# Performance work log

Hardware: AMD Instinct MI355X
Metric: run time of the kernel (lower is better)

The kernel has to match this reference:

```python
import jax, jax.numpy as jnp
import numpy as np

N_NODES = 50000
N_EDGES = 1600000
IN_CH = 128
OUT_SZ = 64


def setup_inputs() -> dict:
    key = jax.random.key(0)
    ks = jax.random.split(key, 10)
    seq = jax.random.normal(ks[0], (N_NODES, IN_CH), dtype=jnp.float32)
    edge_index = jax.random.randint(ks[1], (2, N_EDGES), 0, N_NODES, dtype=jnp.int64)
    s = 1.0 / np.sqrt(IN_CH)
    W_seq = jax.random.uniform(ks[2], (OUT_SZ, IN_CH), jnp.float32, -s, s)
    so = 1.0 / np.sqrt(OUT_SZ)
    w_f1 = jax.random.uniform(ks[3], (OUT_SZ,), jnp.float32, -so, so)
    b_f1 = jax.random.uniform(ks[4], (), jnp.float32, -so, so)
    w_f2 = jax.random.uniform(ks[5], (OUT_SZ,), jnp.float32, -so, so)
    b_f2 = jax.random.uniform(ks[6], (), jnp.float32, -so, so)
    bias = jnp.zeros((OUT_SZ,), jnp.float32)
    W_res = jax.random.uniform(ks[7], (OUT_SZ, IN_CH), jnp.float32, -s, s)
    b_res = jax.random.uniform(ks[8], (OUT_SZ,), jnp.float32, -s, s)
    return {"seq": seq, "edge_index": edge_index, "W_seq": W_seq,
            "w_f1": w_f1, "b_f1": b_f1, "w_f2": w_f2, "b_f2": b_f2,
            "bias": bias, "W_res": W_res, "b_res": b_res}


def reference(seq, edge_index, W_seq, w_f1, b_f1, w_f2, b_f2, bias, W_res, b_res):
    # seq: (N, in_ch); 1x1 conv == linear map per node
    seq_fts = jnp.einsum('ni,oi->no', seq, W_seq)          # (N, out)
    f1 = seq_fts @ w_f1 + b_f1                              # (N,)
    f2 = seq_fts @ w_f2 + b_f2                              # (N,)
    src, dst = edge_index[0], edge_index[1]
    e = jax.nn.leaky_relu(f1[src] + f2[dst], negative_slope=0.01)  # (E,)
    # NOTE: global softmax over all edges, as in the original (not per-node)
    coefs = jax.nn.softmax(e)                               # (E,)
    weighted = coefs[:, None] * seq_fts[dst]                # (E, out)
    vals = jax.ops.segment_sum(weighted, src, num_segments=seq.shape[0])  # (N, out)
    ret = vals + bias
    # residual: in_channel != out_sz -> 1x1 conv with bias
    ret = ret + jnp.einsum('ni,oi->no', seq, W_res) + b_res
    return jax.nn.elu(ret)
```

## Files before the change

kernel.cpp:

```cpp
#include <hip/hip_runtime.h>
#include <hip/hip_bf16.h>
#include <hip/hip_fp8.h>
#include <math.h>

#define N_NODES 50000
#define N_EDGES 1600000
#define IN_CH 128
#define OUT_SZ 64
#define N_TILES 3125

#define NBK 196
#define EPB 4096
#define NBL 391
#define CAP 10240

typedef short bf16x8 __attribute__((ext_vector_type(8)));
typedef float f32x4  __attribute__((ext_vector_type(4)));

__device__ __forceinline__ unsigned fenc(float x) {
    unsigned u = __float_as_uint(x);
    return (u & 0x80000000u) ? ~u : (u | 0x80000000u);
}
__device__ __forceinline__ float fdec(unsigned u) {
    return __uint_as_float((u & 0x80000000u) ? (u & 0x7fffffffu) : ~u);
}

__device__ __forceinline__ short bfbits(float x) {
    union { __hip_bfloat16 h; short s; } u;
    u.h = __float2bfloat16(x);
    return u.s;
}
__device__ __forceinline__ bf16x8 pack8(const float* f) {
    bf16x8 r;
#pragma unroll
    for (int j = 0; j < 8; ++j) r[j] = bfbits(f[j]);
    return r;
}

__global__ __launch_bounds__(256) void k_zero(unsigned* pmax1, unsigned* pmax2,
                                              float* psum, unsigned* bcur) {
    const int t = threadIdx.x;
    if (t < NBK) bcur[t * 16] = (unsigned)t * CAP;
    if (t == 0) { *pmax1 = 0u; *pmax2 = 0u; *psum = 0.0f; }
}

__global__ __launch_bounds__(256) void k_fused(
    const int* __restrict__ ei, unsigned* __restrict__ bcur,
    unsigned* __restrict__ pairs,
    const float* __restrict__ seq, const float* __restrict__ Wseq,
    const float* __restrict__ Wres, const float* __restrict__ wf1,
    const float* __restrict__ bf1, const float* __restrict__ wf2,
    const float* __restrict__ bf2, const float* __restrict__ bias,
    const float* __restrict__ bres,
    __hip_fp8_e4m3* __restrict__ sfp8, float* __restrict__ f1,
    float* __restrict__ f2, unsigned* pmax1, unsigned* pmax2,
    float* __restrict__ out)
{
    __shared__ unsigned buf[EPB];
    __shared__ unsigned hcnt[NBK];
    __shared__ unsigned hoff[NBK];
    __shared__ bf16x8 WL[2048];
    __shared__ float smax[8];
    const int t = threadIdx.x;

    if (blockIdx.x < NBL) {
        const int blk = blockIdx.x;
        if (t < NBK) hcnt[t] = 0u;
        __syncthreads();
#pragma unroll
        for (int k = 0; k < 4; ++k) {
            int idx4 = k * 256 + t;
            int e4 = blk * EPB + idx4 * 4;
            if (e4 < N_EDGES) {
                int4 s = *(const int4*)(ei + e4);
                int4 d = *(const int4*)(ei + N_EDGES + e4);
                buf[k * 1024 + 0 * 256 + t] = ((unsigned)s.x << 16) | (unsigned)d.x;
                buf[k * 1024 + 1 * 256 + t] = ((unsigned)s.y << 16) | (unsigned)d.y;
                buf[k * 1024 + 2 * 256 + t] = ((unsigned)s.z << 16) | (unsigned)d.z;
                buf[k * 1024 + 3 * 256 + t] = ((unsigned)s.w << 16) | (unsigned)d.w;
                atomicAdd(&hcnt[s.x >> 8], 1u);
                atomicAdd(&hcnt[s.y >> 8], 1u);
                atomicAdd(&hcnt[s.z >> 8], 1u);
                atomicAdd(&hcnt[s.w >> 8], 1u);
            }
        }
        __syncthreads();
        if (t < NBK) {
            unsigned c = hcnt[t];
            hoff[t] = c ? atomicAdd(&bcur[t * 16], c) : 0u;
            hcnt[t] = 0u;
        }
        __syncthreads();
#pragma unroll
        for (int k = 0; k < 4; ++k) {
            int idx4 = k * 256 + t;
            int e4 = blk * EPB + idx4 * 4;
            if (e4 < N_EDGES) {
#pragma unroll
                for (int j = 0; j < 4; ++j) {
                    unsigned p = buf[k * 1024 + j * 256 + t];
                    unsigned b = p >> 24;
                    unsigned lp = atomicAdd(&hcnt[b], 1u);
                    pairs[hoff[b] + lp] = p;
                }
            }
        }
        return;
    }

#pragma unroll
    for (int j = 0; j < 8; ++j) {
        int idx = t + j * 256;
        int ct = idx >> 8;
        int ks = (idx >> 6) & 3;
        int li = idx & 63;
        int c = ct * 16 + (li & 15);
        int k0 = ks * 32 + (li >> 4) * 8;
        const float* src = (c < 64) ? (Wseq + c * IN_CH + k0)
                                    : (Wres + (c - 64) * IN_CH + k0);
        float tmp[8];
        *(float4*)tmp = *(const float4*)src;
        *(float4*)(tmp + 4) = *(const float4*)(src + 4);
        WL[idx] = pack8(tmp);
    }
    __syncthreads();

    const int l = t & 63;
    const int wv = t >> 6;
    const int tile = (int)(blockIdx.x - NBL) * 4 + wv;
    const bool active = tile < N_TILES;
    float mx1 = -3.0e38f, mx2 = -3.0e38f;

    if (active) {
        const int row = tile * 16 + (l & 15);
        const int kbase = (l >> 4) * 8;
        f32x4 acc[8];
#pragma unroll
        for (int ct = 0; ct < 8; ++ct) acc[ct] = (f32x4){0.f, 0.f, 0.f, 0.f};

#pragma unroll
        for (int ks = 0; ks < 4; ++ks) {
            const float* ap = seq + (size_t)row * IN_CH + ks * 32 + kbase;
            float tmp[8];
            *(float4*)tmp = *(const float4*)ap;
            *(float4*)(tmp + 4) = *(const float4*)(ap + 4);
            bf16x8 af = pack8(tmp);
#pragma unroll
            for (int ct = 0; ct < 8; ++ct)
                acc[ct] = __builtin_amdgcn_mfma_f32_16x16x32_bf16(
                    af, WL[(ct * 4 + ks) * 64 + l], acc[ct], 0, 0, 0);
        }

        const int n0 = tile * 16;
        float w1v[4], w2v[4], bb[4];
#pragma unroll
        for (int ct = 0; ct < 4; ++ct) {
            int oc = ct * 16 + (l & 15);
            w1v[ct] = wf1[oc];
            w2v[ct] = wf2[oc];
            bb[ct] = bias[oc] + bres[oc];
        }
        const float B1 = bf1[0], B2 = bf2[0];
#pragma unroll
        for (int r = 0; r < 4; ++r) {
            int node = n0 + (l >> 4) * 4 + r;
            size_t o = (size_t)node * 64 + (l & 15);
#pragma unroll
            for (int ct = 0; ct < 4; ++ct) {
                sfp8[o + ct * 16] = __hip_fp8_e4m3(acc[ct][r]);
                out[o + ct * 16] = acc[ct + 4][r] + bb[ct];
            }
            float t1 = acc[0][r] * w1v[0] + acc[1][r] * w1v[1]
                     + acc[2][r] * w1v[2] + acc[3][r] * w1v[3];
            float t2 = acc[0][r] * w2v[0] + acc[1][r] * w2v[1]
                     + acc[2][r] * w2v[2] + acc[3][r] * w2v[3];
#pragma unroll
            for (int m = 8; m; m >>= 1) {
                t1 += __shfl_xor(t1, m);
                t2 += __shfl_xor(t2, m);
            }
            if ((l & 15) == 0) {
                float F1 = t1 + B1, F2 = t2 + B2;
                f1[node] = F1;
                f2[node] = F2;
                mx1 = fmaxf(mx1, F1);
                mx2 = fmaxf(mx2, F2);
            }
        }
    }

    mx1 = fmaxf(mx1, __shfl_xor(mx1, 16)); mx1 = fmaxf(mx1, __shfl_xor(mx1, 32));
    mx2 = fmaxf(mx2, __shfl_xor(mx2, 16)); mx2 = fmaxf(mx2, __shfl_xor(mx2, 32));
    if (l == 0) { smax[wv] = mx1; smax[4 + wv] = mx2; }
    __syncthreads();
    if (t == 0) {
        atomicMax(pmax1, fenc(fmaxf(fmaxf(smax[0], smax[1]), fmaxf(smax[2], smax[3]))));
        atomicMax(pmax2, fenc(fmaxf(fmaxf(smax[4], smax[5]), fmaxf(smax[6], smax[7]))));
    }
}

__global__ __launch_bounds__(1024) void k_sortsum(
    const unsigned* __restrict__ pairs, const unsigned* __restrict__ bcur,
    const float* __restrict__ f1, const float* __restrict__ f2,
    const unsigned* __restrict__ pmax1, const unsigned* __restrict__ pmax2,
    unsigned* __restrict__ offs, unsigned* __restrict__ offsE,
    unsigned* __restrict__ sPair, float* psum)
{
    __shared__ unsigned cur[256];
    __shared__ unsigned bs[256];
    __shared__ float f1loc[256];
    __shared__ float red[16];
    const int t = threadIdx.x;
    const int b = blockIdx.x;
    const int nbase = b << 8;
    const unsigned eb = (unsigned)b * CAP;
    const unsigned ee = bcur[b * 16];

    if (t < 256) {
        cur[t] = 0u;
        int n = nbase + t;
        f1loc[t] = (n < N_NODES) ? f1[n] : 0.f;
    }
    __syncthreads();

    for (unsigned i = eb + t; i < ee; i += 1024)
        atomicAdd(&cur[(pairs[i] >> 16) & 255u], 1u);
    __syncthreads();

    unsigned v = (t < 256) ? cur[t] : 0u;
    if (t < 256) bs[t] = v;
    __syncthreads();
    for (int off = 1; off < 256; off <<= 1) {
        unsigned w = (t >= off && t < 256) ? bs[t - off] : 0u;
        __syncthreads();
        if (t < 256) bs[t] += w;
        __syncthreads();
    }
    if (t < 256) {
        unsigned o = eb + (bs[t] - v);
        int n = nbase + t;
        if (n < N_NODES) { offs[n] = o; offsE[n] = o + v; }
        cur[t] = o;
    }
    __syncthreads();

    float M = fdec(*pmax1) + fdec(*pmax2);
    M = (M > 0.f) ? M : 0.01f * M;
    float ls = 0.f;
    for (unsigned i = eb + t; i < ee; i += 1024) {
        unsigned p = pairs[i];
        unsigned li = (p >> 16) & 255u;
        unsigned dst = p & 0xffffu;
        float x = f1loc[li] + f2[dst];
        x = (x > 0.f) ? x : 0.01f * x;
        float ex = __expf(x - M);
        ls += ex;
        unsigned pos = atomicAdd(&cur[li], 1u);
        sPair[pos] = ((unsigned)(unsigned short)bfbits(ex) << 16) | dst;
    }
#pragma unroll
    for (int off = 32; off; off >>= 1) ls += __shfl_xor(ls, off);
    if ((t & 63) == 0) red[t >> 6] = ls;
    __syncthreads();
    if (t == 0) {
        float bls = 0.f;
#pragma unroll
        for (int k = 0; k < 16; ++k) bls += red[k];
        unsafeAtomicAdd(psum, bls);
    }
}

__global__ __launch_bounds__(256) void k_acc(
    const unsigned* __restrict__ offs, const unsigned* __restrict__ offsE,
    const unsigned* __restrict__ sPair, const __hip_fp8_e4m3* __restrict__ sfp8,
    const float* __restrict__ psum, float* __restrict__ out)
{
    const int lane = threadIdx.x & 63;
    const int n = (blockIdx.x * 256 + threadIdx.x) >> 6;
    if (n >= N_NODES) return;
    const float inv = 1.0f / (*psum);
    const unsigned b = offs[n];
    const unsigned e = offsE[n];

    float acc = 0.f;
    for (unsigned e0 = b; e0 < e; e0 += 64) {
        const int cnt = (int)min(64u, e - e0);
        unsigned p = 0u;
        if (lane < cnt) p = sPair[e0 + lane];
        const int nb = (cnt + 7) & ~7;
        for (int j = 0; j < nb; j += 8) {
            unsigned q0 = __shfl(p, j);
            unsigned q1 = __shfl(p, j + 1);
            unsigned q2 = __shfl(p, j + 2);
            unsigned q3 = __shfl(p, j + 3);
            unsigned q4 = __shfl(p, j + 4);
            unsigned q5 = __shfl(p, j + 5);
            unsigned q6 = __shfl(p, j + 6);
            unsigned q7 = __shfl(p, j + 7);
            float v0 = (float)sfp8[(size_t)(q0 & 0xffffu) * 64 + lane];
            float v1 = (float)sfp8[(size_t)(q1 & 0xffffu) * 64 + lane];
            float v2 = (float)sfp8[(size_t)(q2 & 0xffffu) * 64 + lane];
            float v3 = (float)sfp8[(size_t)(q3 & 0xffffu) * 64 + lane];
            float v4 = (float)sfp8[(size_t)(q4 & 0xffffu) * 64 + lane];
            float v5 = (float)sfp8[(size_t)(q5 & 0xffffu) * 64 + lane];
            float v6 = (float)sfp8[(size_t)(q6 & 0xffffu) * 64 + lane];
            float v7 = (float)sfp8[(size_t)(q7 & 0xffffu) * 64 + lane];
            acc = fmaf(__uint_as_float(q0 & 0xffff0000u), v0, acc);
            acc = fmaf(__uint_as_float(q1 & 0xffff0000u), v1, acc);
            acc = fmaf(__uint_as_float(q2 & 0xffff0000u), v2, acc);
            acc = fmaf(__uint_as_float(q3 & 0xffff0000u), v3, acc);
            acc = fmaf(__uint_as_float(q4 & 0xffff0000u), v4, acc);
            acc = fmaf(__uint_as_float(q5 & 0xffff0000u), v5, acc);
            acc = fmaf(__uint_as_float(q6 & 0xffff0000u), v6, acc);
            acc = fmaf(__uint_as_float(q7 & 0xffff0000u), v7, acc);
        }
    }
    const size_t idx = (size_t)n * 64 + lane;
    float x = out[idx] + acc * inv;
    out[idx] = (x > 0.f) ? x : expm1f(x);
}

extern "C" void kernel_launch(void* const* d_in, const int* in_sizes, int n_in,
                              void* d_out, int out_size, void* d_ws, size_t ws_size,
                              hipStream_t stream) {
    const float* seq  = (const float*)d_in[0];
    const int*   ei   = (const int*)d_in[1];
    const float* Wseq = (const float*)d_in[2];
    const float* wf1  = (const float*)d_in[3];
    const float* bf1  = (const float*)d_in[4];
    const float* wf2  = (const float*)d_in[5];
    const float* bf2  = (const float*)d_in[6];
    const float* bias = (const float*)d_in[7];
    const float* Wres = (const float*)d_in[8];
    const float* bres = (const float*)d_in[9];
    float* out = (float*)d_out;

    unsigned* pmax1     = (unsigned*)d_ws;
    unsigned* pmax2     = (unsigned*)d_ws + 1;
    float*    psum      = (float*)d_ws + 2;
    unsigned* bcur      = (unsigned*)d_ws + 16;
    unsigned* offs      = bcur + NBK * 16;
    unsigned* offsE     = offs + N_NODES;
    unsigned* pairs     = offsE + N_NODES;
    unsigned* sPair     = pairs + (size_t)NBK * CAP;
    __hip_fp8_e4m3* sfp8 = (__hip_fp8_e4m3*)(sPair + (size_t)NBK * CAP);
    float*    f1        = (float*)(sfp8 + (size_t)N_NODES * 64);
    float*    f2        = f1 + N_NODES;

    k_zero<<<1, 256, 0, stream>>>(pmax1, pmax2, psum, bcur);
    k_fused<<<NBL + 782, 256, 0, stream>>>(ei, bcur, pairs,
                                           seq, Wseq, Wres, wf1, bf1, wf2, bf2,
                                           bias, bres, sfp8, f1, f2,
                                           pmax1, pmax2, out);
    k_sortsum<<<NBK, 1024, 0, stream>>>(pairs, bcur, f1, f2, pmax1, pmax2,
                                        offs, offsE, sPair, psum);
    k_acc<<<12500, 256, 0, stream>>>(offs, offsE, sPair, sfp8, psum, out);
}
```

Before: 95.44 us.

## Fuse bucket sort and gather-accumulate into one kernel with grid-wide sum barrier

```diff
diff --git a/kernel.cpp b/kernel.cpp
--- a/kernel.cpp
+++ b/kernel.cpp
@@ -38,10 +38,11 @@
 }
 
 __global__ __launch_bounds__(256) void k_zero(unsigned* pmax1, unsigned* pmax2,
-                                              float* psum, unsigned* bcur) {
+                                              float* psum, unsigned* done,
+                                              unsigned* bcur) {
     const int t = threadIdx.x;
     if (t < NBK) bcur[t * 16] = (unsigned)t * CAP;
-    if (t == 0) { *pmax1 = 0u; *pmax2 = 0u; *psum = 0.0f; }
+    if (t == 0) { *pmax1 = 0u; *pmax2 = 0u; *psum = 0.0f; *done = 0u; }
 }
 
 __global__ __launch_bounds__(256) void k_fused(
@@ -199,22 +200,25 @@
     }
 }
 
-__global__ __launch_bounds__(1024) void k_sortsum(
+__global__ __launch_bounds__(1024) void k_sortacc(
     const unsigned* __restrict__ pairs, const unsigned* __restrict__ bcur,
     const float* __restrict__ f1, const float* __restrict__ f2,
     const unsigned* __restrict__ pmax1, const unsigned* __restrict__ pmax2,
-    unsigned* __restrict__ offs, unsigned* __restrict__ offsE,
-    unsigned* __restrict__ sPair, float* psum)
+    const __hip_fp8_e4m3* __restrict__ sfp8,
+    float* psum, unsigned* done, float* __restrict__ out)
 {
+    __shared__ unsigned sP[CAP];
     __shared__ unsigned cur[256];
+    __shared__ unsigned offsL[256];
     __shared__ unsigned bs[256];
     __shared__ float f1loc[256];
     __shared__ float red[16];
+    __shared__ float sInv;
     const int t = threadIdx.x;
     const int b = blockIdx.x;
     const int nbase = b << 8;
     const unsigned eb = (unsigned)b * CAP;
-    const unsigned ee = bcur[b * 16];
+    const unsigned cnt = bcur[b * 16] - eb;
 
     if (t < 256) {
         cur[t] = 0u;
@@ -223,8 +227,8 @@
     }
     __syncthreads();
 
-    for (unsigned i = eb + t; i < ee; i += 1024)
-        atomicAdd(&cur[(pairs[i] >> 16) & 255u], 1u);
+    for (unsigned i = t; i < cnt; i += 1024)
+        atomicAdd(&cur[(pairs[eb + i] >> 16) & 255u], 1u);
     __syncthreads();
 
     unsigned v = (t < 256) ? cur[t] : 0u;
@@ -237,9 +241,8 @@
         __syncthreads();
     }
     if (t < 256) {
-        unsigned o = eb + (bs[t] - v);
-        int n = nbase + t;
-        if (n < N_NODES) { offs[n] = o; offsE[n] = o + v; }
+        unsigned o = bs[t] - v;
+        offsL[t] = o;
         cur[t] = o;
     }
     __syncthreads();
@@ -247,8 +250,8 @@
     float M = fdec(*pmax1) + fdec(*pmax2);
     M = (M > 0.f) ? M : 0.01f * M;
     float ls = 0.f;
-    for (unsigned i = eb + t; i < ee; i += 1024) {
-        unsigned p = pairs[i];
+    for (unsigned i = t; i < cnt; i += 1024) {
+        unsigned p = pairs[eb + i];
         unsigned li = (p >> 16) & 255u;
         unsigned dst = p & 0xffffu;
         float x = f1loc[li] + f2[dst];
@@ -256,7 +259,7 @@
         float ex = __expf(x - M);
         ls += ex;
         unsigned pos = atomicAdd(&cur[li], 1u);
-        sPair[pos] = ((unsigned)(unsigned short)bfbits(ex) << 16) | dst;
+        sP[pos] = ((unsigned)(unsigned short)bfbits(ex) << 16) | dst;
     }
 #pragma unroll
     for (int off = 32; off; off >>= 1) ls += __shfl_xor(ls, off);
@@ -267,57 +270,68 @@
 #pragma unroll
         for (int k = 0; k < 16; ++k) bls += red[k];
         unsafeAtomicAdd(psum, bls);
-    }
-}
-
-__global__ __launch_bounds__(256) void k_acc(
-    const unsigned* __restrict__ offs, const unsigned* __restrict__ offsE,
-    const unsigned* __restrict__ sPair, const __hip_fp8_e4m3* __restrict__ sfp8,
-    const float* __restrict__ psum, float* __restrict__ out)
-{
-    const int lane = threadIdx.x & 63;
-    const int n = (blockIdx.x * 256 + threadIdx.x) >> 6;
-    if (n >= N_NODES) return;
-    const float inv = 1.0f / (*psum);
-    const unsigned b = offs[n];
-    const unsigned e = offsE[n];
-
-    float acc = 0.f;
-    for (unsigned e0 = b; e0 < e; e0 += 64) {
-        const int cnt = (int)min(64u, e - e0);
-        unsigned p = 0u;
-        if (lane < cnt) p = sPair[e0 + lane];
-        const int nb = (cnt + 7) & ~7;
-        for (int j = 0; j < nb; j += 8) {
-            unsigned q0 = __shfl(p, j);
-            unsigned q1 = __shfl(p, j + 1);
-            unsigned q2 = __shfl(p, j + 2);
-            unsigned q3 = __shfl(p, j + 3);
-            unsigned q4 = __shfl(p, j + 4);
-            unsigned q5 = __shfl(p, j + 5);
-            unsigned q6 = __shfl(p, j + 6);
-            unsigned q7 = __shfl(p, j + 7);
-            float v0 = (float)sfp8[(size_t)(q0 & 0xffffu) * 64 + lane];
-            float v1 = (float)sfp8[(size_t)(q1 & 0xffffu) * 64 + lane];
-            float v2 = (float)sfp8[(size_t)(q2 & 0xffffu) * 64 + lane];
-            float v3 = (float)sfp8[(size_t)(q3 & 0xffffu) * 64 + lane];
-            float v4 = (float)sfp8[(size_t)(q4 & 0xffffu) * 64 + lane];
-            float v5 = (float)sfp8[(size_t)(q5 & 0xffffu) * 64 + lane];
-            float v6 = (float)sfp8[(size_t)(q6 & 0xffffu) * 64 + lane];
-            float v7 = (float)sfp8[(size_t)(q7 & 0xffffu) * 64 + lane];
-            acc = fmaf(__uint_as_float(q0 & 0xffff0000u), v0, acc);
-            acc = fmaf(__uint_as_float(q1 & 0xffff0000u), v1, acc);
-            acc = fmaf(__uint_as_float(q2 & 0xffff0000u), v2, acc);
-            acc = fmaf(__uint_as_float(q3 & 0xffff0000u), v3, acc);
-            acc = fmaf(__uint_as_float(q4 & 0xffff0000u), v4, acc);
-            acc = fmaf(__uint_as_float(q5 & 0xffff0000u), v5, acc);
-            acc = fmaf(__uint_as_float(q6 & 0xffff0000u), v6, acc);
-            acc = fmaf(__uint_as_float(q7 & 0xffff0000u), v7, acc);
-        }
-    }
-    const size_t idx = (size_t)n * 64 + lane;
-    float x = out[idx] + acc * inv;
-    out[idx] = (x > 0.f) ? x : expm1f(x);
+        __threadfence();
+        atomicAdd(done, 1u);
+    }
+
+    const int lane = t & 63;
+    const int wvv = t >> 6;
+    float accv[16];
+#pragma unroll
+    for (int i = 0; i < 16; ++i) {
+        const int ln = wvv * 16 + i;
+        const unsigned s0 = offsL[ln];
+        const unsigned e0 = cur[ln];
+        float acc = 0.f;
+        for (unsigned q = s0; q < e0; q += 64) {
+            const int c = (int)min(64u, e0 - q);
+            unsigned p = (lane < c) ? sP[q + lane] : 0u;
+            const int nb = (c + 7) & ~7;
+            for (int j = 0; j < nb; j += 8) {
+                unsigned q0 = __shfl(p, j);
+                unsigned q1 = __shfl(p, j + 1);
+                unsigned q2 = __shfl(p, j + 2);
+                unsigned q3 = __shfl(p, j + 3);
+                unsigned q4 = __shfl(p, j + 4);
+                unsigned q5 = __shfl(p, j + 5);
+                unsigned q6 = __shfl(p, j + 6);
+                unsigned q7 = __shfl(p, j + 7);
+                float v0 = (float)sfp8[(size_t)(q0 & 0xffffu) * 64 + lane];
+                float v1 = (float)sfp8[(size_t)(q1 & 0xffffu) * 64 + lane];
+                float v2 = (float)sfp8[(size_t)(q2 & 0xffffu) * 64 + lane];
+                float v3 = (float)sfp8[(size_t)(q3 & 0xffffu) * 64 + lane];
+                float v4 = (float)sfp8[(size_t)(q4 & 0xffffu) * 64 + lane];
+                float v5 = (float)sfp8[(size_t)(q5 & 0xffffu) * 64 + lane];
+                float v6 = (float)sfp8[(size_t)(q6 & 0xffffu) * 64 + lane];
+                float v7 = (float)sfp8[(size_t)(q7 & 0xffffu) * 64 + lane];
+                acc = fmaf(__uint_as_float(q0 & 0xffff0000u), v0, acc);
+                acc = fmaf(__uint_as_float(q1 & 0xffff0000u), v1, acc);
+                acc = fmaf(__uint_as_float(q2 & 0xffff0000u), v2, acc);
+                acc = fmaf(__uint_as_float(q3 & 0xffff0000u), v3, acc);
+                acc = fmaf(__uint_as_float(q4 & 0xffff0000u), v4, acc);
+                acc = fmaf(__uint_as_float(q5 & 0xffff0000u), v5, acc);
+                acc = fmaf(__uint_as_float(q6 & 0xffff0000u), v6, acc);
+                acc = fmaf(__uint_as_float(q7 & 0xffff0000u), v7, acc);
+            }
+        }
+        accv[i] = acc;
+    }
+
+    if (t == 0) {
+        while (atomicAdd(done, 0u) < NBK) { }
+        sInv = 1.0f / unsafeAtomicAdd(psum, 0.0f);
+    }
+    __syncthreads();
+    const float inv = sInv;
+#pragma unroll
+    for (int i = 0; i < 16; ++i) {
+        const int n = nbase + wvv * 16 + i;
+        if (n < N_NODES) {
+            const size_t idx = (size_t)n * 64 + lane;
+            float x = out[idx] + accv[i] * inv;
+            out[idx] = (x > 0.f) ? x : expm1f(x);
+        }
+    }
 }
 
 extern "C" void kernel_launch(void* const* d_in, const int* in_sizes, int n_in,
@@ -338,21 +352,18 @@
     unsigned* pmax1     = (unsigned*)d_ws;
     unsigned* pmax2     = (unsigned*)d_ws + 1;
     float*    psum      = (float*)d_ws + 2;
+    unsigned* done      = (unsigned*)d_ws + 3;
     unsigned* bcur      = (unsigned*)d_ws + 16;
-    unsigned* offs      = bcur + NBK * 16;
-    unsigned* offsE     = offs + N_NODES;
-    unsigned* pairs     = offsE + N_NODES;
-    unsigned* sPair     = pairs + (size_t)NBK * CAP;
-    __hip_fp8_e4m3* sfp8 = (__hip_fp8_e4m3*)(sPair + (size_t)NBK * CAP);
+    unsigned* pairs     = bcur + NBK * 16;
+    __hip_fp8_e4m3* sfp8 = (__hip_fp8_e4m3*)(pairs + (size_t)NBK * CAP);
     float*    f1        = (float*)(sfp8 + (size_t)N_NODES * 64);
     float*    f2        = f1 + N_NODES;
 
-    k_zero<<<1, 256, 0, stream>>>(pmax1, pmax2, psum, bcur);
+    k_zero<<<1, 256, 0, stream>>>(pmax1, pmax2, psum, done, bcur);
     k_fused<<<NBL + 782, 256, 0, stream>>>(ei, bcur, pairs,
                                            seq, Wseq, Wres, wf1, bf1, wf2, bf2,
                                            bias, bres, sfp8, f1, f2,
                                            pmax1, pmax2, out);
-    k_sortsum<<<NBK, 1024, 0, stream>>>(pairs, bcur, f1, f2, pmax1, pmax2,
-                                        offs, offsE, sPair, psum);
-    k_acc<<<12500, 256, 0, stream>>>(offs, offsE, sPair, sfp8, psum, out);
-}
+    k_sortacc<<<NBK, 1024, 0, stream>>>(pairs, bcur, f1, f2, pmax1, pmax2,
+                                        sfp8, psum, done, out);
+}
```

After: 113.8 us. 1.19x slower.
